# Kernel optimization log

Hardware: AMD Instinct MI355X
Metric: run time of the kernel (lower is better)

Reference implementation:

```python
import jax, jax.numpy as jnp
import numpy as np

C = 256
HEADS = 4
GROUPS = 8
EPS = 1e-5


def setup_inputs() -> dict:
    key = jax.random.key(0)
    ks = jax.random.split(key, 7)
    B, H, W = 2, 64, 64
    x = jax.random.normal(ks[0], (B, C, H, W), dtype=jnp.float32)
    gamma = jnp.ones((C,), dtype=jnp.float32)
    beta = jnp.zeros((C,), dtype=jnp.float32)
    # conv 1x1 weights stored as [out_ch, in_ch]
    w_qkv = jax.random.normal(ks[1], (3 * C, C), dtype=jnp.float32) * (1.0 / np.sqrt(C))
    b_qkv = jax.random.normal(ks[2], (3 * C,), dtype=jnp.float32) * 0.01
    w_proj = jax.random.normal(ks[3], (C, C), dtype=jnp.float32) * (1.0 / np.sqrt(C))
    b_proj = jax.random.normal(ks[4], (C,), dtype=jnp.float32) * 0.01
    return {"x": x, "gamma": gamma, "beta": beta, "w_qkv": w_qkv,
            "b_qkv": b_qkv, "w_proj": w_proj, "b_proj": b_proj}


def _group_norm(x, gamma, beta):
    B, Cc, H, W = x.shape
    xg = x.reshape(B, GROUPS, Cc // GROUPS, H, W)
    mean = xg.mean(axis=(2, 3, 4), keepdims=True)
    var = xg.var(axis=(2, 3, 4), keepdims=True)
    xg = (xg - mean) * jax.lax.rsqrt(var + EPS)
    xn = xg.reshape(B, Cc, H, W)
    return xn * gamma[None, :, None, None] + beta[None, :, None, None]


def reference(x, gamma, beta, w_qkv, b_qkv, w_proj, b_proj):
    B, Cc, H, W = x.shape
    N = H * W
    hd = Cc // HEADS
    residual = x
    xn = _group_norm(x, gamma, beta)
    # 1x1 conv == channel matmul: [B,3C,H,W]
    qkv = jnp.einsum('oc,bchw->bohw', w_qkv, xn) + b_qkv[None, :, None, None]
    # [B,3,heads,hd,N] -> (3,B,heads,N,hd)
    qkv = qkv.reshape(B, 3, HEADS, hd, N).transpose(1, 0, 2, 4, 3)
    q, k, v = qkv[0], qkv[1], qkv[2]
    scale = hd ** -0.5
    attn = jax.nn.softmax(jnp.einsum('bhnd,bhmd->bhnm', q, k) * scale, axis=-1)
    out = jnp.einsum('bhnm,bhmd->bhnd', attn, v)  # [B,heads,N,hd]
    out = out.transpose(0, 1, 3, 2).reshape(B, Cc, H, W)
    out = jnp.einsum('oc,bchw->bohw', w_proj, out) + b_proj[None, :, None, None]
    return out + residual
```

## Files before the change

kernel.cpp:

```cpp
#include <hip/hip_runtime.h>
#include <stdint.h>

#define EPS 1e-5f

typedef float f32x4 __attribute__((ext_vector_type(4)));
typedef __bf16 bf16x8 __attribute__((ext_vector_type(8)));

__device__ __forceinline__ ushort f2bf(float f){
  union { float f; uint32_t u; } v; v.f = f;
  uint32_t r = v.u + 0x7fffu + ((v.u >> 16) & 1u);
  return (ushort)(r >> 16);
}

__device__ __forceinline__ uint32_t pk2bf(float a, float b){
  __bf16 x = (__bf16)a, y = (__bf16)b;
  return (uint32_t)__builtin_bit_cast(ushort, x) |
         ((uint32_t)__builtin_bit_cast(ushort, y) << 16);
}

__device__ __forceinline__ f32x4 mfma16(bf16x8 a, bf16x8 b, f32x4 c){
  return __builtin_amdgcn_mfma_f32_16x16x32_bf16(a, b, c, 0, 0, 0);
}

__global__ __launch_bounds__(256) void k_prep(const float* wq, const float* wp,
                                              ushort* wqb, ushort* wpb){
  int i = blockIdx.x * 256 + threadIdx.x;
  if (i < 3*256*256) wqb[i] = f2bf(wq[i]);
  if (i < 256*256)   wpb[i] = f2bf(wp[i]);
}

__global__ __launch_bounds__(256) void k_gn1(const float* x, float2* part){
  int bg = blockIdx.x >> 6, pb = blockIdx.x & 63;
  const f32x4* base = (const f32x4*)(x + (size_t)bg*131072 + (size_t)pb*2048);
  float s = 0.f, ss = 0.f;
  #pragma unroll
  for (int it = 0; it < 2; ++it){
    f32x4 v = base[threadIdx.x + it*256];
    #pragma unroll
    for (int j = 0; j < 4; ++j){ s += v[j]; ss += v[j]*v[j]; }
  }
  #pragma unroll
  for (int off = 1; off < 64; off <<= 1){
    s  += __shfl_xor(s,  off);
    ss += __shfl_xor(ss, off);
  }
  __shared__ float red[8];
  int wid = threadIdx.x >> 6;
  if ((threadIdx.x & 63) == 0){ red[wid] = s; red[4 + wid] = ss; }
  __syncthreads();
  if (threadIdx.x == 0){
    part[blockIdx.x] = make_float2(red[0]+red[1]+red[2]+red[3],
                                   red[4]+red[5]+red[6]+red[7]);
  }
}

__global__ __launch_bounds__(64) void k_gn2(const float2* part, float2* stats){
  int bg = blockIdx.x;
  float2 p = part[bg*64 + threadIdx.x];
  float s = p.x, ss = p.y;
  #pragma unroll
  for (int off = 1; off < 64; off <<= 1){
    s  += __shfl_xor(s,  off);
    ss += __shfl_xor(ss, off);
  }
  if (threadIdx.x == 0){
    const float inv = 1.f / 131072.f;
    float mean = s * inv;
    float var  = ss * inv - mean*mean;
    stats[bg] = make_float2(mean, rsqrtf(var + EPS));
  }
}

__global__ __launch_bounds__(256) void k_qkv(const float* x, const float* gamma, const float* beta,
                                             const float2* stats, const ushort* wqb, const float* bqkv,
                                             ushort* Qb, ushort* Kb, ushort* Vb){
  __shared__ ushort A[64][264];
  int b = blockIdx.z, ot = blockIdx.y, nt = blockIdx.x;
  int t = threadIdx.x;
  int nlane = t & 15, cpair = t >> 4;
  int nbase = nt * 64;

  #pragma unroll
  for (int it = 0; it < 8; ++it){
    int c = cpair*2 + it*32;
    float2 st = stats[b*8 + (c >> 5)];
    f32x4 v0 = *(const f32x4*)(x + ((size_t)(b*256 + c    ))*4096 + nbase + nlane*4);
    f32x4 v1 = *(const f32x4*)(x + ((size_t)(b*256 + c + 1))*4096 + nbase + nlane*4);
    float g0 = gamma[c], b0 = beta[c], g1 = gamma[c+1], b1 = beta[c+1];
    #pragma unroll
    for (int j = 0; j < 4; ++j){
      uint32_t lo = f2bf((v0[j] - st.x) * st.y * g0 + b0);
      uint32_t hi = f2bf((v1[j] - st.x) * st.y * g1 + b1);
      *(uint32_t*)&A[nlane*4 + j][c] = lo | (hi << 16);
    }
  }
  __syncthreads();

  int lane = t & 63, wid = t >> 6, l15 = lane & 15, g4 = lane >> 4;
  int o = ot*64 + wid*16 + l15;
  f32x4 acc[4];
  #pragma unroll
  for (int m = 0; m < 4; ++m) acc[m] = (f32x4){0.f,0.f,0.f,0.f};

  #pragma unroll
  for (int ks = 0; ks < 8; ++ks){
    bf16x8 bw = *(const bf16x8*)(wqb + (size_t)o*256 + ks*32 + g4*8);
    #pragma unroll
    for (int mf = 0; mf < 4; ++mf){
      bf16x8 aa = *(const bf16x8*)&A[mf*16 + l15][ks*32 + g4*8];
      acc[mf] = mfma16(aa, bw, acc[mf]);
    }
  }

  int tt = o >> 8, h = (o >> 6) & 3, d = o & 63;
  int bh = b*4 + h;
  float bias = bqkv[o];
  if (tt == 2){
    ushort* dst = Vb + ((size_t)bh*64 + d)*4096;
    #pragma unroll
    for (int mf = 0; mf < 4; ++mf){
      int n0 = nbase + mf*16 + g4*4;
      uint32_t w0 = (uint32_t)f2bf(acc[mf][0]+bias) | ((uint32_t)f2bf(acc[mf][1]+bias) << 16);
      uint32_t w1 = (uint32_t)f2bf(acc[mf][2]+bias) | ((uint32_t)f2bf(acc[mf][3]+bias) << 16);
      *(uint2*)(dst + n0) = make_uint2(w0, w1);
    }
  } else {
    ushort* dst = (tt == 0 ? Qb : Kb) + (size_t)bh*4096*64 + d;
    #pragma unroll
    for (int mf = 0; mf < 4; ++mf){
      int n0 = nbase + mf*16 + g4*4;
      #pragma unroll
      for (int r = 0; r < 4; ++r) dst[(size_t)(n0 + r)*64] = f2bf(acc[mf][r] + bias);
    }
  }
}

__global__ __launch_bounds__(256) void k_attn(const ushort* Qb, const ushort* Kb,
                                              const ushort* Vb, ushort* AO){
  __shared__ ushort Kl[2][64][72];
  __shared__ ushort Vl[2][64][72];
  __shared__ ushort Pl[4][16][72];
  const float SCL2 = 0.125f * 1.44269504f;

  int qt = blockIdx.x, h = blockIdx.y, b = blockIdx.z;
  int bh = b*4 + h;
  int t = threadIdx.x, lane = t & 63, wid = t >> 6, l15 = lane & 15, g4 = lane >> 4;

  const ushort* Qg = Qb + ((size_t)bh*4096 + qt*64 + wid*16 + l15)*64 + g4*8;
  bf16x8 aq0 = *(const bf16x8*)Qg;
  bf16x8 aq1 = *(const bf16x8*)(Qg + 32);

  f32x4 oacc[4];
  #pragma unroll
  for (int m = 0; m < 4; ++m) oacc[m] = (f32x4){0.f,0.f,0.f,0.f};
  float m_s = -INFINITY, l_s = 0.f;

  const ushort* Kgb = Kb + (size_t)bh*4096*64;
  const ushort* Vgb = Vb + (size_t)bh*64*4096;

  {
    int r0 = t >> 3, seg = (t & 7)*8;
    *(uint4*)&Kl[0][r0][seg]      = *(const uint4*)(Kgb + (size_t)r0*64 + seg);
    *(uint4*)&Kl[0][r0+32][seg]   = *(const uint4*)(Kgb + (size_t)(r0+32)*64 + seg);
    *(uint4*)&Vl[0][r0][seg]      = *(const uint4*)(Vgb + (size_t)r0*4096 + seg);
    *(uint4*)&Vl[0][r0+32][seg]   = *(const uint4*)(Vgb + (size_t)(r0+32)*4096 + seg);
  }
  __syncthreads();

  for (int kb = 0; kb < 64; ++kb){
    int cur = kb & 1;
    uint4 kr0, kr1, vr0, vr1;
    int r0 = t >> 3, seg = (t & 7)*8;
    if (kb < 63){
      const ushort* Kg = Kgb + (size_t)(kb+1)*64*64;
      kr0 = *(const uint4*)(Kg + (size_t)r0*64 + seg);
      kr1 = *(const uint4*)(Kg + (size_t)(r0+32)*64 + seg);
      vr0 = *(const uint4*)(Vgb + (size_t)r0*4096 + (kb+1)*64 + seg);
      vr1 = *(const uint4*)(Vgb + (size_t)(r0+32)*4096 + (kb+1)*64 + seg);
    }

    f32x4 s[4];
    #pragma unroll
    for (int m = 0; m < 4; ++m) s[m] = (f32x4){0.f,0.f,0.f,0.f};
    __builtin_amdgcn_s_setprio(1);
    #pragma unroll
    for (int ks = 0; ks < 2; ++ks){
      bf16x8 bq = ks ? aq1 : aq0;
      #pragma unroll
      for (int ct = 0; ct < 4; ++ct){
        bf16x8 kf = *(const bf16x8*)&Kl[cur][ct*16 + l15][ks*32 + g4*8];
        s[ct] = mfma16(kf, bq, s[ct]);
      }
    }
    __builtin_amdgcn_s_setprio(0);

    float vmax = s[0][0];
    #pragma unroll
    for (int ct = 0; ct < 4; ++ct)
      #pragma unroll
      for (int r = 0; r < 4; ++r) vmax = fmaxf(vmax, s[ct][r]);
    vmax = fmaxf(vmax, __shfl_xor(vmax, 16));
    vmax = fmaxf(vmax, __shfl_xor(vmax, 32));
    vmax *= SCL2;
    if (__any(vmax > m_s + 8.f)){
      float mn = fmaxf(m_s, vmax);
      float a = __builtin_amdgcn_exp2f(m_s - mn);
      m_s = mn;
      l_s *= a;
      float ar[4];
      #pragma unroll
      for (int r = 0; r < 4; ++r) ar[r] = __shfl(a, g4*4 + r);
      #pragma unroll
      for (int dt = 0; dt < 4; ++dt)
        #pragma unroll
        for (int r = 0; r < 4; ++r) oacc[dt][r] *= ar[r];
    }
    float rs = 0.f;
    float p[4][4];
    #pragma unroll
    for (int ct = 0; ct < 4; ++ct)
      #pragma unroll
      for (int r = 0; r < 4; ++r){
        float e = __builtin_amdgcn_exp2f(__builtin_fmaf(s[ct][r], SCL2, -m_s));
        p[ct][r] = e; rs += e;
      }
    rs += __shfl_xor(rs, 16);
    rs += __shfl_xor(rs, 32);
    l_s += rs;

    #pragma unroll
    for (int ct = 0; ct < 4; ++ct){
      *(uint32_t*)&Pl[wid][l15][ct*16 + g4*4]     = pk2bf(p[ct][0], p[ct][1]);
      *(uint32_t*)&Pl[wid][l15][ct*16 + g4*4 + 2] = pk2bf(p[ct][2], p[ct][3]);
    }

    __builtin_amdgcn_s_setprio(1);
    #pragma unroll
    for (int ks = 0; ks < 2; ++ks){
      bf16x8 pf = *(const bf16x8*)&Pl[wid][l15][ks*32 + g4*8];
      #pragma unroll
      for (int dt = 0; dt < 4; ++dt){
        bf16x8 vf = *(const bf16x8*)&Vl[cur][dt*16 + l15][ks*32 + g4*8];
        oacc[dt] = mfma16(pf, vf, oacc[dt]);
      }
    }
    __builtin_amdgcn_s_setprio(0);

    if (kb < 63){
      *(uint4*)&Kl[cur^1][r0][seg]    = kr0;
      *(uint4*)&Kl[cur^1][r0+32][seg] = kr1;
      *(uint4*)&Vl[cur^1][r0][seg]    = vr0;
      *(uint4*)&Vl[cur^1][r0+32][seg] = vr1;
      __syncthreads();
    }
  }

  #pragma unroll
  for (int r = 0; r < 4; ++r){
    float lr = __shfl(l_s, g4*4 + r);
    float inv = 1.f / lr;
    int n = qt*64 + wid*16 + g4*4 + r;
    ushort* dst = AO + ((size_t)b*4096 + n)*256 + h*64;
    #pragma unroll
    for (int dt = 0; dt < 4; ++dt)
      dst[dt*16 + l15] = f2bf(oacc[dt][r] * inv);
  }
}

__global__ __launch_bounds__(256) void k_proj(const ushort* AO, const ushort* wpb, const float* bproj,
                                              const float* x, float* out){
  int nt = blockIdx.x, ct = blockIdx.y, b = blockIdx.z;
  int t = threadIdx.x, lane = t & 63, wid = t >> 6, l15 = lane & 15, g4 = lane >> 4;
  int o = ct*64 + wid*16 + l15;
  f32x4 acc[4];
  #pragma unroll
  for (int m = 0; m < 4; ++m) acc[m] = (f32x4){0.f,0.f,0.f,0.f};

  #pragma unroll
  for (int ks = 0; ks < 8; ++ks){
    bf16x8 bw = *(const bf16x8*)(wpb + (size_t)o*256 + ks*32 + g4*8);
    #pragma unroll
    for (int mf = 0; mf < 4; ++mf){
      int n = nt*64 + mf*16 + l15;
      bf16x8 aa = *(const bf16x8*)(AO + ((size_t)b*4096 + n)*256 + ks*32 + g4*8);
      acc[mf] = mfma16(aa, bw, acc[mf]);
    }
  }

  float bias = bproj[o];
  size_t cbase = ((size_t)b*256 + o)*4096;
  #pragma unroll
  for (int mf = 0; mf < 4; ++mf){
    int n0 = nt*64 + mf*16 + g4*4;
    f32x4 res = *(const f32x4*)(x + cbase + n0);
    f32x4 ov;
    #pragma unroll
    for (int r = 0; r < 4; ++r) ov[r] = acc[mf][r] + bias + res[r];
    *(f32x4*)(out + cbase + n0) = ov;
  }
}

extern "C" void kernel_launch(void* const* d_in, const int* in_sizes, int n_in,
                              void* d_out, int out_size, void* d_ws, size_t ws_size,
                              hipStream_t stream) {
  const float* x     = (const float*)d_in[0];
  const float* gamma = (const float*)d_in[1];
  const float* beta  = (const float*)d_in[2];
  const float* wqkv  = (const float*)d_in[3];
  const float* bqkv  = (const float*)d_in[4];
  const float* wproj = (const float*)d_in[5];
  const float* bproj = (const float*)d_in[6];
  float* out = (float*)d_out;

  char* ws = (char*)d_ws;
  float2* part   = (float2*)(ws + 0);
  float2* stats  = (float2*)(ws + 8192);
  ushort* wq_b   = (ushort*)(ws + 16384);
  ushort* wp_b   = (ushort*)(ws + 409600);
  ushort* Qb     = (ushort*)(ws + 1048576);
  ushort* Kb     = (ushort*)(ws + 5242880);
  ushort* Vb     = (ushort*)(ws + 9437184);
  ushort* AO     = (ushort*)(ws + 13631488);

  k_prep<<<768, 256, 0, stream>>>(wqkv, wproj, wq_b, wp_b);
  k_gn1 <<<1024, 256, 0, stream>>>(x, part);
  k_gn2 <<<16, 64, 0, stream>>>(part, stats);
  k_qkv <<<dim3(64,12,2), 256, 0, stream>>>(x, gamma, beta, stats, wq_b, bqkv, Qb, Kb, Vb);
  k_attn<<<dim3(64,4,2), 256, 0, stream>>>(Qb, Kb, Vb, AO);
  k_proj<<<dim3(64,4,2), 256, 0, stream>>>(AO, wp_b, bproj, x, out);
}
```

Baseline: 185.7 us.

## Split attention over KV halves with combine kernel, separate normalization pass

Attention is split along the key dimension into two halves (when workspace allows), doubling workgroup count, and each half writes unnormalized partial outputs plus max/sum stats. A new combine kernel merges the halves. Group-norm finalization moves into a new normalize kernel that writes a bf16 token-major activation. The QKV kernel now reads that activation directly and stages Q/K stores through LDS for coalesced writes. Workgroups are also remapped across XCDs. This adds kernel launches and extra partial-output traffic in exchange for better occupancy in attention and coalesced stores.

```diff
diff --git a/kernel.cpp b/kernel.cpp
--- a/kernel.cpp
+++ b/kernel.cpp
@@ -10,6 +10,11 @@
   union { float f; uint32_t u; } v; v.f = f;
   uint32_t r = v.u + 0x7fffu + ((v.u >> 16) & 1u);
   return (ushort)(r >> 16);
+}
+
+__device__ __forceinline__ float bf2f(ushort u){
+  union { uint32_t u; float f; } v; v.u = ((uint32_t)u) << 16;
+  return v.f;
 }
 
 __device__ __forceinline__ uint32_t pk2bf(float a, float b){
@@ -54,50 +59,60 @@
   }
 }
 
-__global__ __launch_bounds__(64) void k_gn2(const float2* part, float2* stats){
-  int bg = blockIdx.x;
-  float2 p = part[bg*64 + threadIdx.x];
-  float s = p.x, ss = p.y;
-  #pragma unroll
-  for (int off = 1; off < 64; off <<= 1){
-    s  += __shfl_xor(s,  off);
-    ss += __shfl_xor(ss, off);
-  }
-  if (threadIdx.x == 0){
-    const float inv = 1.f / 131072.f;
-    float mean = s * inv;
-    float var  = ss * inv - mean*mean;
-    stats[bg] = make_float2(mean, rsqrtf(var + EPS));
-  }
-}
-
-__global__ __launch_bounds__(256) void k_qkv(const float* x, const float* gamma, const float* beta,
-                                             const float2* stats, const ushort* wqb, const float* bqkv,
+__global__ __launch_bounds__(256) void k_norm(const float* x, const float* gamma, const float* beta,
+                                              const float2* part, ushort* Xn){
+  __shared__ float T[64][65];
+  __shared__ float2 st[2];
+  int nt = blockIdx.x, ct = blockIdx.y, b = blockIdx.z;
+  int t = threadIdx.x, wid = t >> 6, ln = t & 63;
+
+  if (wid < 2){
+    float2 p = part[((b*8) + ct*2 + wid)*64 + ln];
+    float s = p.x, ss = p.y;
+    #pragma unroll
+    for (int off = 1; off < 64; off <<= 1){
+      s  += __shfl_xor(s,  off);
+      ss += __shfl_xor(ss, off);
+    }
+    if (ln == 0){
+      const float inv = 1.f / 131072.f;
+      float mean = s * inv;
+      float var  = ss * inv - mean*mean;
+      st[wid] = make_float2(mean, rsqrtf(var + EPS));
+    }
+  }
+  __syncthreads();
+
+  int c_local = t >> 2, col0 = (t & 3) * 16;
+  float2 s0 = st[c_local >> 5];
+  float g  = gamma[ct*64 + c_local] * s0.y;
+  float bt = beta[ct*64 + c_local] - s0.x * g;
+  const float* xr = x + ((size_t)(b*256 + ct*64 + c_local))*4096 + nt*64 + col0;
+  #pragma unroll
+  for (int j = 0; j < 4; ++j){
+    f32x4 v = *(const f32x4*)(xr + j*4);
+    #pragma unroll
+    for (int e = 0; e < 4; ++e) T[col0 + j*4 + e][c_local] = v[e]*g + bt;
+  }
+  __syncthreads();
+
+  int n_local = t >> 2, c0 = (t & 3) * 16;
+  uint32_t pk[8];
+  #pragma unroll
+  for (int j = 0; j < 8; ++j) pk[j] = pk2bf(T[n_local][c0 + 2*j], T[n_local][c0 + 2*j + 1]);
+  ushort* dst = Xn + ((size_t)b*4096 + nt*64 + n_local)*256 + ct*64 + c0;
+  *(uint4*)dst       = make_uint4(pk[0], pk[1], pk[2], pk[3]);
+  *(uint4*)(dst + 8) = make_uint4(pk[4], pk[5], pk[6], pk[7]);
+}
+
+__global__ __launch_bounds__(256) void k_qkv(const ushort* Xn, const ushort* wqb, const float* bqkv,
                                              ushort* Qb, ushort* Kb, ushort* Vb){
-  __shared__ ushort A[64][264];
-  int b = blockIdx.z, ot = blockIdx.y, nt = blockIdx.x;
-  int t = threadIdx.x;
-  int nlane = t & 15, cpair = t >> 4;
-  int nbase = nt * 64;
-
-  #pragma unroll
-  for (int it = 0; it < 8; ++it){
-    int c = cpair*2 + it*32;
-    float2 st = stats[b*8 + (c >> 5)];
-    f32x4 v0 = *(const f32x4*)(x + ((size_t)(b*256 + c    ))*4096 + nbase + nlane*4);
-    f32x4 v1 = *(const f32x4*)(x + ((size_t)(b*256 + c + 1))*4096 + nbase + nlane*4);
-    float g0 = gamma[c], b0 = beta[c], g1 = gamma[c+1], b1 = beta[c+1];
-    #pragma unroll
-    for (int j = 0; j < 4; ++j){
-      uint32_t lo = f2bf((v0[j] - st.x) * st.y * g0 + b0);
-      uint32_t hi = f2bf((v1[j] - st.x) * st.y * g1 + b1);
-      *(uint32_t*)&A[nlane*4 + j][c] = lo | (hi << 16);
-    }
-  }
-  __syncthreads();
-
-  int lane = t & 63, wid = t >> 6, l15 = lane & 15, g4 = lane >> 4;
+  __shared__ ushort T[64][72];
+  int nt = blockIdx.x, ot = blockIdx.y, b = blockIdx.z;
+  int t = threadIdx.x, lane = t & 63, wid = t >> 6, l15 = lane & 15, g4 = lane >> 4;
   int o = ot*64 + wid*16 + l15;
+  const ushort* A = Xn + ((size_t)b*4096 + nt*64)*256;
+
   f32x4 acc[4];
   #pragma unroll
   for (int m = 0; m < 4; ++m) acc[m] = (f32x4){0.f,0.f,0.f,0.f};
@@ -107,43 +122,54 @@
     bf16x8 bw = *(const bf16x8*)(wqb + (size_t)o*256 + ks*32 + g4*8);
     #pragma unroll
     for (int mf = 0; mf < 4; ++mf){
-      bf16x8 aa = *(const bf16x8*)&A[mf*16 + l15][ks*32 + g4*8];
+      bf16x8 aa = *(const bf16x8*)(A + (size_t)(mf*16 + l15)*256 + ks*32 + g4*8);
       acc[mf] = mfma16(aa, bw, acc[mf]);
     }
   }
 
-  int tt = o >> 8, h = (o >> 6) & 3, d = o & 63;
+  int tt = ot >> 2, h = ot & 3;
   int bh = b*4 + h;
   float bias = bqkv[o];
   if (tt == 2){
+    int d = wid*16 + l15;
     ushort* dst = Vb + ((size_t)bh*64 + d)*4096;
     #pragma unroll
     for (int mf = 0; mf < 4; ++mf){
-      int n0 = nbase + mf*16 + g4*4;
-      uint32_t w0 = (uint32_t)f2bf(acc[mf][0]+bias) | ((uint32_t)f2bf(acc[mf][1]+bias) << 16);
-      uint32_t w1 = (uint32_t)f2bf(acc[mf][2]+bias) | ((uint32_t)f2bf(acc[mf][3]+bias) << 16);
+      int n0 = nt*64 + mf*16 + g4*4;
+      uint32_t w0 = pk2bf(acc[mf][0]+bias, acc[mf][1]+bias);
+      uint32_t w1 = pk2bf(acc[mf][2]+bias, acc[mf][3]+bias);
       *(uint2*)(dst + n0) = make_uint2(w0, w1);
     }
   } else {
-    ushort* dst = (tt == 0 ? Qb : Kb) + (size_t)bh*4096*64 + d;
-    #pragma unroll
-    for (int mf = 0; mf < 4; ++mf){
-      int n0 = nbase + mf*16 + g4*4;
-      #pragma unroll
-      for (int r = 0; r < 4; ++r) dst[(size_t)(n0 + r)*64] = f2bf(acc[mf][r] + bias);
-    }
-  }
-}
-
+    int d = wid*16 + l15;
+    #pragma unroll
+    for (int mf = 0; mf < 4; ++mf)
+      #pragma unroll
+      for (int r = 0; r < 4; ++r)
+        T[mf*16 + g4*4 + r][d] = f2bf(acc[mf][r] + bias);
+    __syncthreads();
+    int n_local = t >> 2, d0 = (t & 3) * 16;
+    ushort* dst = (tt == 0 ? Qb : Kb) + ((size_t)bh*4096 + nt*64 + n_local)*64 + d0;
+    *(uint4*)dst       = *(uint4*)&T[n_local][d0];
+    *(uint4*)(dst + 8) = *(uint4*)&T[n_local][d0 + 8];
+  }
+}
+
+template<int SPLIT>
 __global__ __launch_bounds__(256) void k_attn(const ushort* Qb, const ushort* Kb,
-                                              const ushort* Vb, ushort* AO){
+                                              const ushort* Vb, ushort* Opart, float2* ML){
   __shared__ ushort Kl[2][64][72];
   __shared__ ushort Vl[2][64][72];
   __shared__ ushort Pl[4][16][72];
   const float SCL2 = 0.125f * 1.44269504f;
 
-  int qt = blockIdx.x, h = blockIdx.y, b = blockIdx.z;
-  int bh = b*4 + h;
+  int nwg = 512*SPLIT;
+  int w = (blockIdx.x & 7) * (nwg >> 3) + (blockIdx.x >> 3);
+  int per_bh = 64*SPLIT;
+  int bh = w / per_bh, rem = w % per_bh;
+  int qt = rem & 63, half = rem >> 6;
+  int b = bh >> 2;
+
   int t = threadIdx.x, lane = t & 63, wid = t >> 6, l15 = lane & 15, g4 = lane >> 4;
 
   const ushort* Qg = Qb + ((size_t)bh*4096 + qt*64 + wid*16 + l15)*64 + g4*8;
@@ -158,20 +184,23 @@
   const ushort* Kgb = Kb + (size_t)bh*4096*64;
   const ushort* Vgb = Vb + (size_t)bh*64*4096;
 
+  const int iters = 64 / SPLIT;
+  const int kb0 = half * iters, kbEnd = kb0 + iters;
+
+  int r0 = t >> 3, seg = (t & 7)*8;
   {
-    int r0 = t >> 3, seg = (t & 7)*8;
-    *(uint4*)&Kl[0][r0][seg]      = *(const uint4*)(Kgb + (size_t)r0*64 + seg);
-    *(uint4*)&Kl[0][r0+32][seg]   = *(const uint4*)(Kgb + (size_t)(r0+32)*64 + seg);
-    *(uint4*)&Vl[0][r0][seg]      = *(const uint4*)(Vgb + (size_t)r0*4096 + seg);
-    *(uint4*)&Vl[0][r0+32][seg]   = *(const uint4*)(Vgb + (size_t)(r0+32)*4096 + seg);
+    const ushort* Kg = Kgb + (size_t)kb0*64*64;
+    *(uint4*)&Kl[0][r0][seg]    = *(const uint4*)(Kg + (size_t)r0*64 + seg);
+    *(uint4*)&Kl[0][r0+32][seg] = *(const uint4*)(Kg + (size_t)(r0+32)*64 + seg);
+    *(uint4*)&Vl[0][r0][seg]    = *(const uint4*)(Vgb + (size_t)r0*4096 + kb0*64 + seg);
+    *(uint4*)&Vl[0][r0+32][seg] = *(const uint4*)(Vgb + (size_t)(r0+32)*4096 + kb0*64 + seg);
   }
   __syncthreads();
 
-  for (int kb = 0; kb < 64; ++kb){
+  for (int kb = kb0; kb < kbEnd; ++kb){
     int cur = kb & 1;
     uint4 kr0, kr1, vr0, vr1;
-    int r0 = t >> 3, seg = (t & 7)*8;
-    if (kb < 63){
+    if (kb < kbEnd - 1){
       const ushort* Kg = Kgb + (size_t)(kb+1)*64*64;
       kr0 = *(const uint4*)(Kg + (size_t)r0*64 + seg);
       kr1 = *(const uint4*)(Kg + (size_t)(r0+32)*64 + seg);
@@ -194,11 +223,11 @@
     }
     __builtin_amdgcn_s_setprio(0);
 
-    float vmax = s[0][0];
-    #pragma unroll
-    for (int ct = 0; ct < 4; ++ct)
-      #pragma unroll
-      for (int r = 0; r < 4; ++r) vmax = fmaxf(vmax, s[ct][r]);
+    float v01 = fmaxf(fmaxf(s[0][0], s[0][1]), fmaxf(s[0][2], s[0][3]));
+    float v23 = fmaxf(fmaxf(s[1][0], s[1][1]), fmaxf(s[1][2], s[1][3]));
+    float v45 = fmaxf(fmaxf(s[2][0], s[2][1]), fmaxf(s[2][2], s[2][3]));
+    float v67 = fmaxf(fmaxf(s[3][0], s[3][1]), fmaxf(s[3][2], s[3][3]));
+    float vmax = fmaxf(fmaxf(v01, v23), fmaxf(v45, v67));
     vmax = fmaxf(vmax, __shfl_xor(vmax, 16));
     vmax = fmaxf(vmax, __shfl_xor(vmax, 32));
     vmax *= SCL2;
@@ -246,7 +275,7 @@
     }
     __builtin_amdgcn_s_setprio(0);
 
-    if (kb < 63){
+    if (kb < kbEnd - 1){
       *(uint4*)&Kl[cur^1][r0][seg]    = kr0;
       *(uint4*)&Kl[cur^1][r0+32][seg] = kr1;
       *(uint4*)&Vl[cur^1][r0][seg]    = vr0;
@@ -255,16 +284,65 @@
     }
   }
 
+  int pb = (bh*SPLIT + half)*64 + qt;
+  if (g4 == 0) ML[(size_t)pb*64 + wid*16 + l15] = make_float2(m_s, l_s);
+  ushort* dst = Opart + (size_t)pb*4096;
   #pragma unroll
   for (int r = 0; r < 4; ++r){
-    float lr = __shfl(l_s, g4*4 + r);
-    float inv = 1.f / lr;
-    int n = qt*64 + wid*16 + g4*4 + r;
-    ushort* dst = AO + ((size_t)b*4096 + n)*256 + h*64;
+    int n_local = wid*16 + g4*4 + r;
     #pragma unroll
     for (int dt = 0; dt < 4; ++dt)
-      dst[dt*16 + l15] = f2bf(oacc[dt][r] * inv);
-  }
+      dst[(size_t)n_local*64 + dt*16 + l15] = f2bf(oacc[dt][r]);
+  }
+}
+
+template<int SPLIT>
+__global__ __launch_bounds__(256) void k_comb(const ushort* Opart, const float2* ML, ushort* AO){
+  int qt = blockIdx.x, bh = blockIdx.y;
+  int b = bh >> 2, h = bh & 3;
+  int t = threadIdx.x, n_local = t >> 2, d0 = (t & 3) * 16;
+  int pb1 = (bh*SPLIT)*64 + qt;
+  float2 ml1 = ML[(size_t)pb1*64 + n_local];
+  const ushort* o1 = Opart + (size_t)pb1*4096 + n_local*64 + d0;
+  ushort* dst = AO + ((size_t)b*4096 + qt*64 + n_local)*256 + h*64 + d0;
+
+  uint4 a0 = *(const uint4*)o1;
+  uint4 a1 = *(const uint4*)(o1 + 8);
+  const ushort* u1 = (const ushort*)&a0;
+  uint32_t pk[8];
+  if (SPLIT == 1){
+    float inv = 1.f / ml1.y;
+    float vals[16];
+    #pragma unroll
+    for (int j = 0; j < 8; ++j) vals[j]   = bf2f(((const ushort*)&a0)[j]) * inv;
+    #pragma unroll
+    for (int j = 0; j < 8; ++j) vals[j+8] = bf2f(((const ushort*)&a1)[j]) * inv;
+    #pragma unroll
+    for (int j = 0; j < 8; ++j) pk[j] = pk2bf(vals[2*j], vals[2*j+1]);
+  } else {
+    int pb2 = pb1 + 64;
+    float2 ml2 = ML[(size_t)pb2*64 + n_local];
+    const ushort* o2 = Opart + (size_t)pb2*4096 + n_local*64 + d0;
+    uint4 b0 = *(const uint4*)o2;
+    uint4 b1 = *(const uint4*)(o2 + 8);
+    float m  = fmaxf(ml1.x, ml2.x);
+    float e1 = __builtin_amdgcn_exp2f(ml1.x - m);
+    float e2 = __builtin_amdgcn_exp2f(ml2.x - m);
+    float inv = 1.f / (ml1.y*e1 + ml2.y*e2);
+    float f1 = e1 * inv, f2 = e2 * inv;
+    float vals[16];
+    #pragma unroll
+    for (int j = 0; j < 8; ++j)
+      vals[j]   = bf2f(((const ushort*)&a0)[j])*f1 + bf2f(((const ushort*)&b0)[j])*f2;
+    #pragma unroll
+    for (int j = 0; j < 8; ++j)
+      vals[j+8] = bf2f(((const ushort*)&a1)[j])*f1 + bf2f(((const ushort*)&b1)[j])*f2;
+    #pragma unroll
+    for (int j = 0; j < 8; ++j) pk[j] = pk2bf(vals[2*j], vals[2*j+1]);
+  }
+  (void)u1;
+  *(uint4*)dst       = make_uint4(pk[0], pk[1], pk[2], pk[3]);
+  *(uint4*)(dst + 8) = make_uint4(pk[4], pk[5], pk[6], pk[7]);
 }
 
 __global__ __launch_bounds__(256) void k_proj(const ushort* AO, const ushort* wpb, const float* bproj,
@@ -312,20 +390,30 @@
   const float* bproj = (const float*)d_in[6];
   float* out = (float*)d_out;
 
+  const size_t MiB = 1024*1024;
   char* ws = (char*)d_ws;
   float2* part   = (float2*)(ws + 0);
-  float2* stats  = (float2*)(ws + 8192);
   ushort* wq_b   = (ushort*)(ws + 16384);
   ushort* wp_b   = (ushort*)(ws + 409600);
-  ushort* Qb     = (ushort*)(ws + 1048576);
-  ushort* Kb     = (ushort*)(ws + 5242880);
-  ushort* Vb     = (ushort*)(ws + 9437184);
-  ushort* AO     = (ushort*)(ws + 13631488);
+  ushort* Qb     = (ushort*)(ws + 1*MiB);
+  ushort* Kb     = (ushort*)(ws + 5*MiB);
+  ushort* Vb     = (ushort*)(ws + 9*MiB);
+  ushort* Xn     = (ushort*)(ws + 13*MiB);
+  ushort* AO     = (ushort*)(ws + 13*MiB);
+  ushort* Opart  = (ushort*)(ws + 17*MiB);
+  int split = (ws_size >= 27*MiB) ? 2 : 1;
+  float2* ML     = (float2*)(ws + (17 + 4*(size_t)split)*MiB);
 
   k_prep<<<768, 256, 0, stream>>>(wqkv, wproj, wq_b, wp_b);
   k_gn1 <<<1024, 256, 0, stream>>>(x, part);
-  k_gn2 <<<16, 64, 0, stream>>>(part, stats);
-  k_qkv <<<dim3(64,12,2), 256, 0, stream>>>(x, gamma, beta, stats, wq_b, bqkv, Qb, Kb, Vb);
-  k_attn<<<dim3(64,4,2), 256, 0, stream>>>(Qb, Kb, Vb, AO);
+  k_norm<<<dim3(64,4,2), 256, 0, stream>>>(x, gamma, beta, part, Xn);
+  k_qkv <<<dim3(64,12,2), 256, 0, stream>>>(Xn, wq_b, bqkv, Qb, Kb, Vb);
+  if (split == 2){
+    k_attn<2><<<1024, 256, 0, stream>>>(Qb, Kb, Vb, Opart, ML);
+    k_comb<2><<<dim3(64,8), 256, 0, stream>>>(Opart, ML, AO);
+  } else {
+    k_attn<1><<<512, 256, 0, stream>>>(Qb, Kb, Vb, Opart, ML);
+    k_comb<1><<<dim3(64,8), 256, 0, stream>>>(Opart, ML, AO);
+  }
   k_proj<<<dim3(64,4,2), 256, 0, stream>>>(AO, wp_b, bproj, x, out);
 }
```

Measured after the change: 219.8 us. 1.18x slower.
